# Kernel optimization log

Measured on AMD Instinct MI355X. Metric: run time of the kernel, lower is better.

## Reference

```python
import jax, jax.numpy as jnp
import numpy as np


def dht(x):
    # Discrete Hartley transform along last axis: DHT(x) = Re(FFT) - Im(FFT)
    X = jnp.fft.fft(x, axis=-1)
    return (X.real - X.imag).astype(x.dtype)


def idht(x):
    # Inverse DHT = DHT / N
    n = x.shape[-1]
    return dht(x) / n


def setup_inputs() -> dict:
    key = jax.random.key(0)
    k1, k2 = jax.random.split(key)
    B, Cin, Cout, N, M = 16, 64, 64, 16384, 64
    x = jax.random.normal(k1, (B, Cin, N), dtype=jnp.float32)
    scale = 1.0 / (Cin * Cout)
    weights1 = scale * jax.random.uniform(k2, (Cout, Cin, M), dtype=jnp.float32)
    return {"x": x, "weights1": weights1, "modes1": M}


def reference(x, weights1, modes1):
    # x: [B, Cin, N]; weights1: [Cout, Cin, M]
    B, Cin, N = x.shape
    Cout = weights1.shape[0]
    x_ht = dht(x)                                  # [B, Cin, N]
    # Mode-wise channel contraction on the first `modes1` Hartley modes
    low = jnp.einsum('bim,oim->bom', x_ht[:, :, :modes1], weights1)  # [B, Cout, M]
    out_ht = jnp.zeros((B, Cout, N), dtype=x.dtype).at[:, :, :modes1].set(low)
    return idht(out_ht)                            # [B, Cout, N]
```

## Files before the change

kernel.cpp:

```cpp
#include <hip/hip_runtime.h>
#include <math.h>

#define N_FFT 16384
#define HALF 8192
#define ROWS 1024
#define KS_A 64
#define KR_A 128
#define CHUNK 32
#define NMASK 16383


__global__ __launch_bounds__(256) void k_tab(float* __restrict__ castab,
                                             float* __restrict__ costab) {
    int i = blockIdx.x * 256 + threadIdx.x;
    double ang = 6.283185307179586476925287 * (double)i / (double)N_FFT;
    double c = cos(ang), s = sin(ang);
    castab[i] = (float)(c + s);
    costab[i] = (float)(2.0 * c);
}

__global__ __launch_bounds__(512, 4) void kA(const float* __restrict__ x,
                                             const float* __restrict__ castab,
                                             const float* __restrict__ costab,
                                             float* __restrict__ partial) {
    const int rb = blockIdx.x & 7;
    const int ks = blockIdx.x >> 3;
    const int rowbase = rb << 7;
    const int kbase = ks * KR_A;

    __shared__ float xs[CHUNK][2][128];

    const int t   = threadIdx.x;
    const int wq  = __builtin_amdgcn_readfirstlane(t >> 6);
    const int lam = t & 63;
    const int c0  = wq * 8;
    const int p   = wq >> 2;
    const int r2  = lam * 2;
    const int mbase = (wq < 4) ? (wq << 4) : (((wq - 4) << 4) + 1);

    float k2[8], cA[8], cB[8];
#pragma unroll
    for (int j = 0; j < 8; ++j) {
        const int m = mbase + 2 * j;
        k2[j] = costab[m];
        cB[j] = castab[((kbase - 1) * m) & NMASK];
        cA[j] = castab[(kbase * m) & NMASK];
    }

    float acc0[8], acc1[8];
#pragma unroll
    for (int j = 0; j < 8; ++j) { acc0[j] = 0.f; acc1[j] = 0.f; }

    for (int ch = 0; ch < KR_A / CHUNK; ++ch) {
        const int k0 = kbase + ch * CHUNK;
        if (ch) __syncthreads();
#pragma unroll
        for (int it = 0; it < 2; ++it) {
            const int idx = it * 512 + t;
            const int r = idx >> 3, kq = idx & 7;
            const float4 a4 = *reinterpret_cast<const float4*>(
                &x[(size_t)(rowbase + r) * N_FFT + k0 + kq * 4]);
            const float4 b4 = *reinterpret_cast<const float4*>(
                &x[(size_t)(rowbase + r) * N_FFT + k0 + kq * 4 + HALF]);
            const int rsw = r ^ (kq << 1);
#pragma unroll
            for (int u = 0; u < 4; ++u) {
                const float a = reinterpret_cast<const float*>(&a4)[u];
                const float b = reinterpret_cast<const float*>(&b4)[u];
                xs[kq * 4 + u][0][rsw] = a + b;
                xs[kq * 4 + u][1][rsw] = a - b;
            }
        }
        __syncthreads();

        for (int k = 0; k < CHUNK; k += 2) {
            {
                const int rd = r2 ^ ((k >> 2) << 1);
                const float2 s2 = *reinterpret_cast<const float2*>(&xs[k][p][rd]);
#pragma unroll
                for (int j = 0; j < 8; ++j) {
                    acc0[j] = fmaf(s2.x, cA[j], acc0[j]);
                    acc1[j] = fmaf(s2.y, cA[j], acc1[j]);
                    cB[j] = fmaf(k2[j], cA[j], -cB[j]);
                }
            }
            {
                const int rd = r2 ^ (((k + 1) >> 2) << 1);
                const float2 s2 = *reinterpret_cast<const float2*>(&xs[k + 1][p][rd]);
#pragma unroll
                for (int j = 0; j < 8; ++j) {
                    acc0[j] = fmaf(s2.x, cB[j], acc0[j]);
                    acc1[j] = fmaf(s2.y, cB[j], acc1[j]);
                    cA[j] = fmaf(k2[j], cB[j], -cA[j]);
                }
            }
        }
    }

#pragma unroll
    for (int i = 0; i < 2; ++i) {
        float* pp = &partial[((size_t)ks << 16) +
                             (size_t)(rowbase + r2 + i) * 64 + c0];
        const float* a = i ? acc1 : acc0;
        *reinterpret_cast<float4*>(pp) =
            make_float4(a[0], a[1], a[2], a[3]);
        *reinterpret_cast<float4*>(pp + 4) =
            make_float4(a[4], a[5], a[6], a[7]);
    }
}

__global__ __launch_bounds__(256) void kR(const float* __restrict__ partial,
                                          float* __restrict__ xh) {
    const int idx = blockIdx.x * 256 + threadIdx.x;
    const int r = idx >> 6, c = idx & 63;
    const int m = (c < 32) ? (2 * c) : (2 * (c - 32) + 1);
    float a0 = 0.f, a1 = 0.f, a2 = 0.f, a3 = 0.f;
#pragma unroll 4
    for (int sp = 0; sp < KS_A; sp += 4) {
        a0 += partial[((size_t)(sp + 0) << 16) + idx];
        a1 += partial[((size_t)(sp + 1) << 16) + idx];
        a2 += partial[((size_t)(sp + 2) << 16) + idx];
        a3 += partial[((size_t)(sp + 3) << 16) + idx];
    }
    xh[(r << 6) + m] = (a0 + a1) + (a2 + a3);
}

__global__ __launch_bounds__(256) void kB(const float* __restrict__ xh,
                                          const float* __restrict__ w,
                                          float* __restrict__ lowT) {
    const int b  = blockIdx.x >> 4;
    const int og = blockIdx.x & 15;
    const int o  = og * 4 + (threadIdx.x >> 6);
    const int m  = threadIdx.x & 63;
    float a0 = 0.f, a1 = 0.f, a2 = 0.f, a3 = 0.f;
#pragma unroll 4
    for (int i = 0; i < 64; i += 4) {
        a0 = fmaf(xh[(size_t)((b * 64 + i + 0) << 6) + m], w[(size_t)((o * 64 + i + 0) << 6) + m], a0);
        a1 = fmaf(xh[(size_t)((b * 64 + i + 1) << 6) + m], w[(size_t)((o * 64 + i + 1) << 6) + m], a1);
        a2 = fmaf(xh[(size_t)((b * 64 + i + 2) << 6) + m], w[(size_t)((o * 64 + i + 2) << 6) + m], a2);
        a3 = fmaf(xh[(size_t)((b * 64 + i + 3) << 6) + m], w[(size_t)((o * 64 + i + 3) << 6) + m], a3);
    }
    lowT[(size_t)m * ROWS + b * 64 + o] = ((a0 + a1) + (a2 + a3)) * (1.0f / (float)N_FFT);
}

__global__ __launch_bounds__(256, 4) void kC(const float* __restrict__ lowT,
                                             const float* __restrict__ castab,
                                             const float* __restrict__ costab,
                                             float* __restrict__ out) {
    const int nb = blockIdx.x & 127;
    const int rb = blockIdx.x >> 7;
    const int t  = threadIdx.x;
    const int wq = __builtin_amdgcn_readfirstlane(t >> 6);
    const int r0 = rb * 64 + wq * 16;
    const int n  = (nb << 6) + (t & 63);

    const float k2 = costab[n];
    float ce = 1.0f;
    float co = castab[n];

    float se[16], so[16];
#pragma unroll
    for (int j = 0; j < 16; ++j) { se[j] = 0.f; so[j] = 0.f; }

#pragma unroll 2
    for (int g = 0; g < 32; ++g) {
        const float* le = lowT + ((size_t)(2 * g) << 10) + r0;
        const float* lo = le + ROWS;
#pragma unroll
        for (int j = 0; j < 16; ++j) {
            se[j] = fmaf(ce, le[j], se[j]);
            so[j] = fmaf(co, lo[j], so[j]);
        }
        ce = fmaf(k2, co, -ce);
        co = fmaf(k2, ce, -co);
    }

#pragma unroll
    for (int j = 0; j < 16; ++j) {
        const size_t row = (size_t)r0 + j;
        out[row * N_FFT + n]        = se[j] + so[j];
        out[row * N_FFT + HALF + n] = se[j] - so[j];
    }
}

extern "C" void kernel_launch(void* const* d_in, const int* in_sizes, int n_in,
                              void* d_out, int out_size, void* d_ws, size_t ws_size,
                              hipStream_t stream) {
    const float* x = (const float*)d_in[0];
    const float* w = (const float*)d_in[1];
    float* out = (float*)d_out;
    float* ws  = (float*)d_ws;

    float* castab  = ws;
    float* costab  = ws + 16384;
    float* partial = ws + 32768;
    float* xh      = ws + 4227072;
    float* lowT    = ws + 4292608;

    k_tab<<<64, 256, 0, stream>>>(castab, costab);
    kA<<<512, 512, 0, stream>>>(x, castab, costab, partial);
    kR<<<256, 256, 0, stream>>>(partial, xh);
    kB<<<256, 256, 0, stream>>>(xh, w, lowT);
    kC<<<2048, 256, 0, stream>>>(lowT, castab, costab, out);
}
```

Measured before the change: 66.86 us.

## Prefetch next chunk in kA, split reductions in kR/kB, nontemporal I/O

kA now loads 64-column chunks with nontemporal vector loads and prefetches the second chunk into registers while the first is being processed, using a wider LDS swizzle. kR and kB each split their reduction across more blocks and waves, combining the pieces through shared memory, so small reduction kernels get more parallelism. kC unrolls its mode loop further and writes output with nontemporal stores to avoid polluting the cache. The register prefetch raises VGPR pressure in kA, and the doubled CHUNK doubles its LDS footprint, both of which may reduce occupancy.

```diff
diff --git a/kernel.cpp b/kernel.cpp
--- a/kernel.cpp
+++ b/kernel.cpp
@@ -6,8 +6,10 @@
 #define ROWS 1024
 #define KS_A 64
 #define KR_A 128
-#define CHUNK 32
+#define CHUNK 64
 #define NMASK 16383
+
+typedef float float4n __attribute__((ext_vector_type(4)));
 
 
 __global__ __launch_bounds__(256) void k_tab(float* __restrict__ castab,
@@ -51,31 +53,45 @@
 #pragma unroll
     for (int j = 0; j < 8; ++j) { acc0[j] = 0.f; acc1[j] = 0.f; }
 
-    for (int ch = 0; ch < KR_A / CHUNK; ++ch) {
-        const int k0 = kbase + ch * CHUNK;
+    float4n xa[4], xb[4];
+
+#define LOADCH(K0)                                                            \
+    _Pragma("unroll")                                                         \
+    for (int it = 0; it < 4; ++it) {                                          \
+        const int idx = it * 512 + t;                                         \
+        const int r = idx >> 4, kq = idx & 15;                                \
+        const float* src = &x[(size_t)(rowbase + r) * N_FFT + (K0) + kq * 4]; \
+        xa[it] = __builtin_nontemporal_load(                                  \
+            reinterpret_cast<const float4n*>(src));                           \
+        xb[it] = __builtin_nontemporal_load(                                  \
+            reinterpret_cast<const float4n*>(src + HALF));                    \
+    }
+
+#define WRITECH()                                                             \
+    _Pragma("unroll")                                                         \
+    for (int it = 0; it < 4; ++it) {                                          \
+        const int idx = it * 512 + t;                                         \
+        const int r = idx >> 4, kq = idx & 15;                                \
+        const int rsw = r ^ (kq << 2);                                        \
+        _Pragma("unroll")                                                     \
+        for (int u = 0; u < 4; ++u) {                                         \
+            const float a = xa[it][u];                                        \
+            const float b = xb[it][u];                                        \
+            xs[kq * 4 + u][0][rsw] = a + b;                                   \
+            xs[kq * 4 + u][1][rsw] = a - b;                                   \
+        }                                                                     \
+    }
+
+    LOADCH(kbase);
+    for (int ch = 0; ch < 2; ++ch) {
         if (ch) __syncthreads();
-#pragma unroll
-        for (int it = 0; it < 2; ++it) {
-            const int idx = it * 512 + t;
-            const int r = idx >> 3, kq = idx & 7;
-            const float4 a4 = *reinterpret_cast<const float4*>(
-                &x[(size_t)(rowbase + r) * N_FFT + k0 + kq * 4]);
-            const float4 b4 = *reinterpret_cast<const float4*>(
-                &x[(size_t)(rowbase + r) * N_FFT + k0 + kq * 4 + HALF]);
-            const int rsw = r ^ (kq << 1);
-#pragma unroll
-            for (int u = 0; u < 4; ++u) {
-                const float a = reinterpret_cast<const float*>(&a4)[u];
-                const float b = reinterpret_cast<const float*>(&b4)[u];
-                xs[kq * 4 + u][0][rsw] = a + b;
-                xs[kq * 4 + u][1][rsw] = a - b;
-            }
-        }
+        WRITECH();
         __syncthreads();
-
+        if (ch == 0) { LOADCH(kbase + CHUNK); }
+#pragma unroll 4
         for (int k = 0; k < CHUNK; k += 2) {
+            const int rd = r2 ^ ((k >> 2) << 2);
             {
-                const int rd = r2 ^ ((k >> 2) << 1);
                 const float2 s2 = *reinterpret_cast<const float2*>(&xs[k][p][rd]);
 #pragma unroll
                 for (int j = 0; j < 8; ++j) {
@@ -85,7 +101,6 @@
                 }
             }
             {
-                const int rd = r2 ^ (((k + 1) >> 2) << 1);
                 const float2 s2 = *reinterpret_cast<const float2*>(&xs[k + 1][p][rd]);
 #pragma unroll
                 for (int j = 0; j < 8; ++j) {
@@ -96,6 +111,8 @@
             }
         }
     }
+#undef LOADCH
+#undef WRITECH
 
 #pragma unroll
     for (int i = 0; i < 2; ++i) {
@@ -111,36 +128,62 @@
 
 __global__ __launch_bounds__(256) void kR(const float* __restrict__ partial,
                                           float* __restrict__ xh) {
-    const int idx = blockIdx.x * 256 + threadIdx.x;
-    const int r = idx >> 6, c = idx & 63;
-    const int m = (c < 32) ? (2 * c) : (2 * (c - 32) + 1);
+    const int lane = threadIdx.x & 63;
+    const int sg   = threadIdx.x >> 6;
+    const int idx  = blockIdx.x * 64 + lane;
+    const int sp0  = sg << 4;
+
     float a0 = 0.f, a1 = 0.f, a2 = 0.f, a3 = 0.f;
-#pragma unroll 4
-    for (int sp = 0; sp < KS_A; sp += 4) {
-        a0 += partial[((size_t)(sp + 0) << 16) + idx];
-        a1 += partial[((size_t)(sp + 1) << 16) + idx];
-        a2 += partial[((size_t)(sp + 2) << 16) + idx];
-        a3 += partial[((size_t)(sp + 3) << 16) + idx];
-    }
-    xh[(r << 6) + m] = (a0 + a1) + (a2 + a3);
+#pragma unroll
+    for (int i = 0; i < 16; i += 4) {
+        a0 += partial[((size_t)(sp0 + i + 0) << 16) + idx];
+        a1 += partial[((size_t)(sp0 + i + 1) << 16) + idx];
+        a2 += partial[((size_t)(sp0 + i + 2) << 16) + idx];
+        a3 += partial[((size_t)(sp0 + i + 3) << 16) + idx];
+    }
+    const float s = (a0 + a1) + (a2 + a3);
+
+    __shared__ float red[4][64];
+    red[sg][lane] = s;
+    __syncthreads();
+    if (sg == 0) {
+        const float v = (red[0][lane] + red[1][lane]) +
+                        (red[2][lane] + red[3][lane]);
+        const int r = idx >> 6, c = idx & 63;
+        const int m = (c < 32) ? (2 * c) : (2 * (c - 32) + 1);
+        xh[(r << 6) + m] = v;
+    }
 }
 
 __global__ __launch_bounds__(256) void kB(const float* __restrict__ xh,
                                           const float* __restrict__ w,
                                           float* __restrict__ lowT) {
-    const int b  = blockIdx.x >> 4;
-    const int og = blockIdx.x & 15;
-    const int o  = og * 4 + (threadIdx.x >> 6);
+    const int b  = blockIdx.x >> 5;
+    const int op = blockIdx.x & 31;
     const int m  = threadIdx.x & 63;
+    const int oo = (threadIdx.x >> 6) & 1;
+    const int ih = threadIdx.x >> 7;
+    const int o  = op * 2 + oo;
+    const int i0 = ih * 32;
+
     float a0 = 0.f, a1 = 0.f, a2 = 0.f, a3 = 0.f;
-#pragma unroll 4
-    for (int i = 0; i < 64; i += 4) {
+#pragma unroll
+    for (int ii = 0; ii < 32; ii += 4) {
+        const int i = i0 + ii;
         a0 = fmaf(xh[(size_t)((b * 64 + i + 0) << 6) + m], w[(size_t)((o * 64 + i + 0) << 6) + m], a0);
         a1 = fmaf(xh[(size_t)((b * 64 + i + 1) << 6) + m], w[(size_t)((o * 64 + i + 1) << 6) + m], a1);
         a2 = fmaf(xh[(size_t)((b * 64 + i + 2) << 6) + m], w[(size_t)((o * 64 + i + 2) << 6) + m], a2);
         a3 = fmaf(xh[(size_t)((b * 64 + i + 3) << 6) + m], w[(size_t)((o * 64 + i + 3) << 6) + m], a3);
     }
-    lowT[(size_t)m * ROWS + b * 64 + o] = ((a0 + a1) + (a2 + a3)) * (1.0f / (float)N_FFT);
+    const float s = (a0 + a1) + (a2 + a3);
+
+    __shared__ float red[2][128];
+    red[ih][oo * 64 + m] = s;
+    __syncthreads();
+    if (ih == 0) {
+        lowT[(size_t)m * ROWS + b * 64 + o] =
+            (s + red[1][oo * 64 + m]) * (1.0f / (float)N_FFT);
+    }
 }
 
 __global__ __launch_bounds__(256, 4) void kC(const float* __restrict__ lowT,
@@ -162,7 +205,7 @@
 #pragma unroll
     for (int j = 0; j < 16; ++j) { se[j] = 0.f; so[j] = 0.f; }
 
-#pragma unroll 2
+#pragma unroll 4
     for (int g = 0; g < 32; ++g) {
         const float* le = lowT + ((size_t)(2 * g) << 10) + r0;
         const float* lo = le + ROWS;
@@ -178,8 +221,8 @@
 #pragma unroll
     for (int j = 0; j < 16; ++j) {
         const size_t row = (size_t)r0 + j;
-        out[row * N_FFT + n]        = se[j] + so[j];
-        out[row * N_FFT + HALF + n] = se[j] - so[j];
+        __builtin_nontemporal_store(se[j] + so[j], &out[row * N_FFT + n]);
+        __builtin_nontemporal_store(se[j] - so[j], &out[row * N_FFT + HALF + n]);
     }
 }
 
@@ -199,7 +242,7 @@
 
     k_tab<<<64, 256, 0, stream>>>(castab, costab);
     kA<<<512, 512, 0, stream>>>(x, castab, costab, partial);
-    kR<<<256, 256, 0, stream>>>(partial, xh);
-    kB<<<256, 256, 0, stream>>>(xh, w, lowT);
+    kR<<<1024, 256, 0, stream>>>(partial, xh);
+    kB<<<512, 256, 0, stream>>>(xh, w, lowT);
     kC<<<2048, 256, 0, stream>>>(lowT, castab, costab, out);
 }
```

After: 71.69 us. 1.07x slower.
